# Kernel tuning notes

Hardware: AMD Instinct MI355X
Metric: run time of the kernel (lower is better)

The kernel has to match this reference:

```python
import jax, jax.numpy as jnp
import numpy as np
import math

IN_F, OUT_F = 4096, 4096
ORDER, TENSOR_RANK = 4, 8
LEAF_A = math.ceil(IN_F ** (1.0 / ORDER))   # 8
LEAF_B = math.ceil(OUT_F ** (1.0 / ORDER))  # 8


def setup_inputs() -> dict:
    key = jax.random.key(0)
    k1, k2, k3, k4 = jax.random.split(key, 4)
    x = jax.random.normal(k1, (8, 2048, IN_F), dtype=jnp.float32)
    weight = jax.random.normal(k2, (OUT_F, IN_F), dtype=jnp.float32) * 0.02
    bias = jax.random.normal(k3, (OUT_F,), dtype=jnp.float32) * 0.02
    # reset_parameters: gain for leaky_relu(sqrt(5)) = sqrt(2/(1+5)); std = gain / in_features**(1/order)
    gain = math.sqrt(2.0 / (1.0 + 5.0))
    std = gain / (IN_F ** (1.0 / ORDER))
    weight_leafs = jax.random.uniform(
        k4, (ORDER, TENSOR_RANK, LEAF_A, LEAF_B), dtype=jnp.float32,
        minval=-std, maxval=std)
    return {"x": x, "weight": weight, "bias": bias, "weight_leafs": weight_leafs}


def _reproduce_weight(weight_leafs):
    # Original einsum 'lij,rmn->rimjn' sums the FIRST operand over its leading
    # (rank) axis; chained through both stages + final .sum(0), every leaf is
    # summed over tensor_rank. Exact math = nested Kronecker of the rank-summed
    # leaves, sliced to [:in_features, :out_features].
    s = weight_leafs.sum(axis=1)  # (4, a, b)
    a, b = LEAF_A, LEAF_B
    z1 = jnp.einsum('ij,mn->imjn', s[0], s[1]).reshape(a * a, b * b)
    z2 = jnp.einsum('ij,mn->imjn', s[2], s[3]).reshape(a * a, b * b)
    zzz = jnp.einsum('ij,mn->imjn', z1, z2).reshape(a ** 4, b ** 4)
    return zzz[:IN_F, :OUT_F]  # (in_features, out_features)


def reference(x, weight, bias, weight_leafs):
    tensor_weight = _reproduce_weight(weight_leafs)       # (in, out)
    full_weight = weight + tensor_weight.T                # (out, in)
    # F.linear: x @ W^T + b
    return jnp.einsum('bsi,oi->bso', x, full_weight) + bias
```

## Files before the change

### kernel.cpp

```cpp
#include <hip/hip_runtime.h>
#include <hip/hip_bf16.h>
#include <stdint.h>

typedef __attribute__((ext_vector_type(8)))  __bf16 bf16x8;
typedef __attribute__((ext_vector_type(4)))  float  f32x4;
typedef __attribute__((ext_vector_type(16))) float  f32x16;

#define IN_F   4096
#define OUT_F  4096
#define M_ROWS 16384

static __device__ __forceinline__ unsigned short f2bf(float f) {
    unsigned int u = __float_as_uint(f);
    u += 0x7FFFu + ((u >> 16) & 1u);
    return (unsigned short)(u >> 16);
}

#define PREP_WBLK 1366
#define PREP_NBLK 4096

__global__ __launch_bounds__(256) void prep_kernel(
    const float* __restrict__ weight, const float* __restrict__ leafs,
    const float* __restrict__ x,
    unsigned short* __restrict__ wb, unsigned short* __restrict__ xbuf)
{
    const int t = threadIdx.x;
    if (blockIdx.x < PREP_WBLK) {
        __shared__ float s[4][8][8];
        {
            const int o = t >> 6, a = (t >> 3) & 7, b = t & 7;
            float acc = 0.f;
            #pragma unroll
            for (int r = 0; r < 8; ++r)
                acc += leafs[o * 512 + r * 64 + a * 8 + b];
            s[o][a][b] = acc;
        }
        __syncthreads();

        const int total = (OUT_F * IN_F) / 8;
        for (int idx = blockIdx.x * 256 + t; idx < total; idx += PREP_WBLK * 256) {
            const int n  = idx >> 9;
            const int kg = idx & 511;
            const int n0 = n >> 9, n1 = (n >> 6) & 7, n2 = (n >> 3) & 7, n3 = n & 7;
            const int k0 = kg >> 6, k1 = (kg >> 3) & 7, k2 = kg & 7;
            const float p = s[0][k0][n0] * s[1][k1][n1] * s[2][k2][n2];
            const float4* wp = (const float4*)(weight + (size_t)n * IN_F + kg * 8);
            const float4 w0 = wp[0], w1 = wp[1];
            const float wv[8] = {w0.x, w0.y, w0.z, w0.w, w1.x, w1.y, w1.z, w1.w};
            unsigned int pk[4];
            #pragma unroll
            for (int j = 0; j < 4; ++j) {
                unsigned int lo = f2bf(wv[2*j]   + p * s[3][2*j]  [n3]);
                unsigned int hi = f2bf(wv[2*j+1] + p * s[3][2*j+1][n3]);
                pk[j] = lo | (hi << 16);
            }
            *reinterpret_cast<uint4*>(wb + (size_t)n * IN_F + kg * 8) =
                make_uint4(pk[0], pk[1], pk[2], pk[3]);
        }
    } else {
        const long long n8 = (long long)M_ROWS * IN_F / 8;
        const int xblocks = PREP_NBLK - PREP_WBLK;
        for (long long idx = (long long)(blockIdx.x - PREP_WBLK) * 256 + t;
             idx < n8; idx += (long long)xblocks * 256) {
            const float4* xp = (const float4*)(x + idx * 8);
            const float4 a = xp[0], b = xp[1];
            const float v[8] = {a.x, a.y, a.z, a.w, b.x, b.y, b.z, b.w};
            unsigned int pk[4];
            #pragma unroll
            for (int j = 0; j < 4; ++j)
                pk[j] = (unsigned int)f2bf(v[2*j]) | ((unsigned int)f2bf(v[2*j+1]) << 16);
            *reinterpret_cast<uint4*>(xbuf + idx * 8) =
                make_uint4(pk[0], pk[1], pk[2], pk[3]);
        }
    }
}

#define BK 64
#define NT 64

#define GLL(src, dst) __builtin_amdgcn_global_load_lds( \
    (const __attribute__((address_space(1))) void*)(src), \
    (__attribute__((address_space(3))) void*)(dst), 16, 0, 0)

#define SB0  __builtin_amdgcn_sched_barrier(0)
#define BAR  __builtin_amdgcn_s_barrier()
#define PRI1 __builtin_amdgcn_s_setprio(1)
#define PRI0 __builtin_amdgcn_s_setprio(0)
#define WLG0 asm volatile("s_waitcnt lgkmcnt(0)" ::: "memory")
#define WVM0 asm volatile("s_waitcnt vmcnt(0)" ::: "memory")

#define STAGE_A(b, h, ko) do { \
    GLL(pA[h] + (ko),             ldsb + (b)*32768 + (h)*16384 + t*16); \
    GLL(pA[h] + 64*IN_F + (ko),   ldsb + (b)*32768 + (h)*16384 + t*16 + 8192); } while(0)
#define STAGE_B(b, h, ko) do { \
    GLL(pB[h] + (ko),             ldsb + 65536 + (b)*32768 + (h)*16384 + t*16); \
    GLL(pB[h] + 64*IN_F + (ko),   ldsb + 65536 + (b)*32768 + (h)*16384 + t*16 + 8192); } while(0)

#define ARD(Q, KH) do { _Pragma("unroll") \
    for (int i_ = 0; i_ < 2; ++i_) { _Pragma("unroll") \
    for (int j_ = 0; j_ < 2; ++j_) \
        aF[i_][j_] = *(const bf16x8*)(aPan + ((Q)*2 + i_)*4096 + \
                     (aOff ^ ((((KH)*2 + j_)) << 5))); } } while(0)
#define BRD(KH) do { _Pragma("unroll") \
    for (int n_ = 0; n_ < 2; ++n_) { _Pragma("unroll") \
    for (int j_ = 0; j_ < 2; ++j_) \
        bFr[n_][j_] = *(const bf16x8*)(bPan + n_*4096 + \
                      (bOff ^ ((((KH)*2 + j_)) << 5))); } } while(0)
#define MM32(Q) do { _Pragma("unroll") \
    for (int i_ = 0; i_ < 2; ++i_) { _Pragma("unroll") \
    for (int n_ = 0; n_ < 2; ++n_) { _Pragma("unroll") \
    for (int j_ = 0; j_ < 2; ++j_) \
        acc[(Q)*2 + i_][n_] = __builtin_amdgcn_mfma_f32_32x32x16_bf16( \
            aF[i_][j_], bFr[n_][j_], acc[(Q)*2 + i_][n_], 0, 0, 0); } } } while(0)

#define TILE32(BUF, KO, PF) do { \
    const char* aPan = ldsb + (BUF)*32768 + wr*16384; \
    const char* bPan = ldsb + 65536 + (BUF)*32768 + (wcn >> 1)*16384; \
     \
    ARD(0, 0); BRD(0); \
    if (PF) { STAGE_A((BUF)^1, 0, KO); STAGE_A((BUF)^1, 1, KO); } \
    BAR; WLG0; SB0; PRI1; MM32(0); PRI0; BAR; \
     \
    ARD(1, 0); \
    if (PF) { STAGE_B((BUF)^1, 0, KO); STAGE_B((BUF)^1, 1, KO); } \
    BAR; WLG0; SB0; PRI1; MM32(1); PRI0; BAR; \
     \
    ARD(0, 1); BRD(1); \
    BAR; WLG0; SB0; PRI1; MM32(0); PRI0; BAR; \
     \
    ARD(1, 1); \
    BAR; WLG0; SB0; PRI1; MM32(1); PRI0; \
    if (PF) { WVM0; } \
    BAR; \
} while (0)

__global__ __launch_bounds__(512, 2) void gemm32_kernel(
    const unsigned short* __restrict__ xb,
    const unsigned short* __restrict__ wb,
    const float* __restrict__ bias,
    float* __restrict__ out)
{
    __shared__ unsigned short lds_us[65536];
    char* const ldsb = (char*)lds_us;

    const int t    = threadIdx.x;
    const int wave = t >> 6;
    const int lane = t & 63;
    const int ln31 = lane & 31;
    const int lhi  = lane >> 5;
    const int wr   = wave >> 2;
    const int wcn  = wave & 3;

    const int bid  = blockIdx.x;
    const int swzb = (bid & 7) * 128 + (bid >> 3);
    const int bm   = (swzb >> 4) * 256;
    const int bn   = (swzb & 15) * 256;

    const int r1  = t >> 3;
    const int slp = (t & 7) ^ (r1 & 7);
    const unsigned short* pA[2] = {
        xb + (size_t)(bm + r1) * IN_F + slp * 8,
        xb + (size_t)(bm + 128 + r1) * IN_F + slp * 8 };
    const unsigned short* pB[2] = {
        wb + (size_t)(bn + r1) * IN_F + slp * 8,
        wb + (size_t)(bn + 128 + r1) * IN_F + slp * 8 };

    const int c0   = ((lhi ^ (ln31 & 7)) << 4);
    const int aOff = ln31 * 128 + c0;
    const int bOff = ((wcn & 1) * 64 + ln31) * 128 + c0;

    f32x16 acc[4][2] = {};
    bf16x8 aF[2][2], bFr[2][2];

    STAGE_A(0, 0, 0); STAGE_A(0, 1, 0); STAGE_B(0, 0, 0); STAGE_B(0, 1, 0);
    WVM0; BAR;

    #pragma unroll 1
    for (int tt = 0; tt < NT - 2; tt += 2) {
        TILE32(0, (tt + 1) * BK, true);
        TILE32(1, (tt + 2) * BK, true);
    }
    TILE32(0, (NT - 1) * BK, true);
    TILE32(1, 0, false);

    #pragma unroll
    for (int fn = 0; fn < 2; ++fn) {
        const int col = bn + wcn * 64 + fn * 32 + ln31;
        const float bv = bias[col];
        #pragma unroll
        for (int fm = 0; fm < 4; ++fm) {
            const int rb = bm + wr * 128 + fm * 32 + 4 * lhi;
            #pragma unroll
            for (int reg = 0; reg < 16; ++reg) {
                const int row = rb + (reg & 3) + 8 * (reg >> 2);
                out[(size_t)row * OUT_F + col] = acc[fm][fn][reg] + bv;
            }
        }
    }
}

#define FBM 128
#define FBN 128
#define FBK 32

__global__ __launch_bounds__(256) void gemm_fb_kernel(
    const float* __restrict__ xf,
    const unsigned short* __restrict__ wb,
    const float* __restrict__ bias,
    float* __restrict__ out)
{
    __shared__ unsigned short As[FBM * FBK];
    __shared__ unsigned short Bs[FBN * FBK];

    const int t    = threadIdx.x;
    const int wave = t >> 6;
    const int lane = t & 63;
    const int lr   = lane & 15;
    const int kq   = lane >> 4;
    const int wr   = wave >> 1;
    const int wc   = wave & 1;

    const int bm = blockIdx.x * FBM;
    const int bn = blockIdx.y * FBN;
    const int srow = t >> 2;
    const int scol = (t & 3) * 8;

    f32x4 acc[4][4] = {};

    for (int kt = 0; kt < IN_F; kt += FBK) {
        #pragma unroll
        for (int g = 0; g < 2; ++g) {
            const int row = srow + g * 64;
            const float4* xp = (const float4*)(xf + (size_t)(bm + row) * IN_F + kt + scol);
            const float4 a0 = xp[0], a1 = xp[1];
            const float v[8] = {a0.x, a0.y, a0.z, a0.w, a1.x, a1.y, a1.z, a1.w};
            unsigned int pk[4];
            #pragma unroll
            for (int j = 0; j < 4; ++j)
                pk[j] = (unsigned int)f2bf(v[2*j]) | ((unsigned int)f2bf(v[2*j+1]) << 16);
            *reinterpret_cast<uint4*>(&As[row * FBK + scol]) =
                make_uint4(pk[0], pk[1], pk[2], pk[3]);
        }
        {
            const unsigned short* gb0 = wb + (size_t)(bn + srow) * IN_F + kt + scol;
            const unsigned short* gb1 = gb0 + (size_t)64 * IN_F;
            GLL(gb0, Bs + srow * FBK + scol);
            GLL(gb1, Bs + (64 + srow) * FBK + scol);
        }
        __syncthreads();

        bf16x8 af[4], bfr[4];
        #pragma unroll
        for (int m = 0; m < 4; ++m)
            af[m] = *reinterpret_cast<const bf16x8*>(As + (wr * 64 + m * 16 + lr) * FBK + kq * 8);
        #pragma unroll
        for (int n = 0; n < 4; ++n)
            bfr[n] = *reinterpret_cast<const bf16x8*>(Bs + (wc * 64 + n * 16 + lr) * FBK + kq * 8);

        #pragma unroll
        for (int m = 0; m < 4; ++m)
            #pragma unroll
            for (int n = 0; n < 4; ++n)
                acc[m][n] = __builtin_amdgcn_mfma_f32_16x16x32_bf16(af[m], bfr[n], acc[m][n], 0, 0, 0);

        __syncthreads();
    }

    const int crow0 = kq * 4;
    #pragma unroll
    for (int n = 0; n < 4; ++n) {
        const int col = bn + wc * 64 + n * 16 + lr;
        const float bv = bias[col];
        #pragma unroll
        for (int m = 0; m < 4; ++m) {
            const int rowb = bm + wr * 64 + m * 16 + crow0;
            #pragma unroll
            for (int j = 0; j < 4; ++j)
                out[(size_t)(rowb + j) * OUT_F + col] = acc[m][n][j] + bv;
        }
    }
}

extern "C" void kernel_launch(void* const* d_in, const int* in_sizes, int n_in,
                              void* d_out, int out_size, void* d_ws, size_t ws_size,
                              hipStream_t stream) {
    const float* x      = (const float*)d_in[0];
    const float* weight = (const float*)d_in[1];
    const float* bias   = (const float*)d_in[2];
    const float* leafs  = (const float*)d_in[3];
    float* out = (float*)d_out;

    unsigned short* wb = (unsigned short*)d_ws;
    unsigned short* xbuf = (unsigned short*)((char*)d_ws +
                           (size_t)OUT_F * IN_F * sizeof(unsigned short));

    const size_t need_full = (size_t)OUT_F * IN_F * 2 + (size_t)M_ROWS * IN_F * 2;
    const bool full = ws_size >= need_full;

    if (full) {
        prep_kernel<<<dim3(PREP_NBLK), dim3(256), 0, stream>>>(
            weight, leafs, x, wb, xbuf);
        gemm32_kernel<<<dim3((M_ROWS / 256) * (OUT_F / 256)), dim3(512), 0, stream>>>(
            xbuf, wb, bias, out);
    } else {
        prep_kernel<<<dim3(PREP_WBLK), dim3(256), 0, stream>>>(
            weight, leafs, x, wb, xbuf);
        gemm_fb_kernel<<<dim3(M_ROWS / FBM, OUT_F / FBN), dim3(256), 0, stream>>>(
            x, wb, bias, out);
    }
}
```

Baseline: 616.1 us.

## Restructure bf16 GEMM main loop around K-slab LDS layout with one barrier per tile

Replaces the hand-scheduled TILE32 pipeline with a simpler double-buffered loop. That loop used XOR-swizzled LDS panels, several barriers per tile and explicit waitcnt and sched barriers. The new loop stores each 64-wide K tile as four 16-element K slabs (32 bytes per row) and issues the next tile's global-to-LDS loads up front. It then runs 4 K-steps of 4x2 MFMAs with only one __syncthreads per tile. The aim is to cut barrier and scheduling overhead and simplify LDS fragment addressing. The cost is that global loads now fetch only 32 contiguous bytes per row, and overlap relies on the compiler's implicit waits instead of explicit vmcnt control.

```diff
diff --git a/kernel.cpp b/kernel.cpp
--- a/kernel.cpp
+++ b/kernel.cpp
@@ -82,59 +82,13 @@
     (const __attribute__((address_space(1))) void*)(src), \
     (__attribute__((address_space(3))) void*)(dst), 16, 0, 0)
 
-#define SB0  __builtin_amdgcn_sched_barrier(0)
-#define BAR  __builtin_amdgcn_s_barrier()
-#define PRI1 __builtin_amdgcn_s_setprio(1)
-#define PRI0 __builtin_amdgcn_s_setprio(0)
-#define WLG0 asm volatile("s_waitcnt lgkmcnt(0)" ::: "memory")
-#define WVM0 asm volatile("s_waitcnt vmcnt(0)" ::: "memory")
-
-#define STAGE_A(b, h, ko) do { \
-    GLL(pA[h] + (ko),             ldsb + (b)*32768 + (h)*16384 + t*16); \
-    GLL(pA[h] + 64*IN_F + (ko),   ldsb + (b)*32768 + (h)*16384 + t*16 + 8192); } while(0)
-#define STAGE_B(b, h, ko) do { \
-    GLL(pB[h] + (ko),             ldsb + 65536 + (b)*32768 + (h)*16384 + t*16); \
-    GLL(pB[h] + 64*IN_F + (ko),   ldsb + 65536 + (b)*32768 + (h)*16384 + t*16 + 8192); } while(0)
-
-#define ARD(Q, KH) do { _Pragma("unroll") \
-    for (int i_ = 0; i_ < 2; ++i_) { _Pragma("unroll") \
-    for (int j_ = 0; j_ < 2; ++j_) \
-        aF[i_][j_] = *(const bf16x8*)(aPan + ((Q)*2 + i_)*4096 + \
-                     (aOff ^ ((((KH)*2 + j_)) << 5))); } } while(0)
-#define BRD(KH) do { _Pragma("unroll") \
-    for (int n_ = 0; n_ < 2; ++n_) { _Pragma("unroll") \
-    for (int j_ = 0; j_ < 2; ++j_) \
-        bFr[n_][j_] = *(const bf16x8*)(bPan + n_*4096 + \
-                      (bOff ^ ((((KH)*2 + j_)) << 5))); } } while(0)
-#define MM32(Q) do { _Pragma("unroll") \
-    for (int i_ = 0; i_ < 2; ++i_) { _Pragma("unroll") \
-    for (int n_ = 0; n_ < 2; ++n_) { _Pragma("unroll") \
-    for (int j_ = 0; j_ < 2; ++j_) \
-        acc[(Q)*2 + i_][n_] = __builtin_amdgcn_mfma_f32_32x32x16_bf16( \
-            aF[i_][j_], bFr[n_][j_], acc[(Q)*2 + i_][n_], 0, 0, 0); } } } while(0)
-
-#define TILE32(BUF, KO, PF) do { \
-    const char* aPan = ldsb + (BUF)*32768 + wr*16384; \
-    const char* bPan = ldsb + 65536 + (BUF)*32768 + (wcn >> 1)*16384; \
-     \
-    ARD(0, 0); BRD(0); \
-    if (PF) { STAGE_A((BUF)^1, 0, KO); STAGE_A((BUF)^1, 1, KO); } \
-    BAR; WLG0; SB0; PRI1; MM32(0); PRI0; BAR; \
-     \
-    ARD(1, 0); \
-    if (PF) { STAGE_B((BUF)^1, 0, KO); STAGE_B((BUF)^1, 1, KO); } \
-    BAR; WLG0; SB0; PRI1; MM32(1); PRI0; BAR; \
-     \
-    ARD(0, 1); BRD(1); \
-    BAR; WLG0; SB0; PRI1; MM32(0); PRI0; BAR; \
-     \
-    ARD(1, 1); \
-    BAR; WLG0; SB0; PRI1; MM32(1); PRI0; \
-    if (PF) { WVM0; } \
-    BAR; \
-} while (0)
-
-__global__ __launch_bounds__(512, 2) void gemm32_kernel(
+#define STAGE(P, KO) do { _Pragma("unroll") \
+    for (int i_ = 0; i_ < 4; ++i_) { \
+        GLL(srcA + (KO) + i_ * 16, ldsb + (P)*65536 + t*16 + i_*8192); \
+        GLL(srcB + (KO) + i_ * 16, ldsb + (P)*65536 + 32768 + t*16 + i_*8192); \
+    } } while (0)
+
+__global__ __launch_bounds__(512, 2) void gemm32k_kernel(
     const unsigned short* __restrict__ xb,
     const unsigned short* __restrict__ wb,
     const float* __restrict__ bias,
@@ -156,32 +110,45 @@
     const int bm   = (swzb >> 4) * 256;
     const int bn   = (swzb & 15) * 256;
 
-    const int r1  = t >> 3;
-    const int slp = (t & 7) ^ (r1 & 7);
-    const unsigned short* pA[2] = {
-        xb + (size_t)(bm + r1) * IN_F + slp * 8,
-        xb + (size_t)(bm + 128 + r1) * IN_F + slp * 8 };
-    const unsigned short* pB[2] = {
-        wb + (size_t)(bn + r1) * IN_F + slp * 8,
-        wb + (size_t)(bn + 128 + r1) * IN_F + slp * 8 };
-
-    const int c0   = ((lhi ^ (ln31 & 7)) << 4);
-    const int aOff = ln31 * 128 + c0;
-    const int bOff = ((wcn & 1) * 64 + ln31) * 128 + c0;
+    const unsigned short* srcA =
+        xb + (size_t)(bm + ((t >> 1) & 255)) * IN_F + (t & 1) * 8;
+    const unsigned short* srcB =
+        wb + (size_t)(bn + ((t >> 1) & 255)) * IN_F + (t & 1) * 8;
+
+    const int aOff = (wr * 128 + ln31) * 32 + lhi * 16;
+    const int bOff = 32768 + (wcn * 64 + ln31) * 32 + lhi * 16;
 
     f32x16 acc[4][2] = {};
-    bf16x8 aF[2][2], bFr[2][2];
-
-    STAGE_A(0, 0, 0); STAGE_A(0, 1, 0); STAGE_B(0, 0, 0); STAGE_B(0, 1, 0);
-    WVM0; BAR;
+
+    STAGE(0, 0);
+    __syncthreads();
 
     #pragma unroll 1
-    for (int tt = 0; tt < NT - 2; tt += 2) {
-        TILE32(0, (tt + 1) * BK, true);
-        TILE32(1, (tt + 2) * BK, true);
-    }
-    TILE32(0, (NT - 1) * BK, true);
-    TILE32(1, 0, false);
+    for (int tt = 0; tt < NT; ++tt) {
+        const int p = tt & 1;
+        if (tt + 1 < NT) STAGE(p ^ 1, (tt + 1) * BK);
+
+        const char* pan = ldsb + p * 65536;
+        __builtin_amdgcn_s_setprio(1);
+        #pragma unroll
+        for (int ks = 0; ks < 4; ++ks) {
+            bf16x8 a[4], b[2];
+            #pragma unroll
+            for (int m = 0; m < 4; ++m)
+                a[m] = *(const bf16x8*)(pan + ks * 8192 + aOff + m * 1024);
+            #pragma unroll
+            for (int n = 0; n < 2; ++n)
+                b[n] = *(const bf16x8*)(pan + ks * 8192 + bOff + n * 1024);
+            #pragma unroll
+            for (int m = 0; m < 4; ++m)
+                #pragma unroll
+                for (int n = 0; n < 2; ++n)
+                    acc[m][n] = __builtin_amdgcn_mfma_f32_32x32x16_bf16(
+                        a[m], b[n], acc[m][n], 0, 0, 0);
+        }
+        __builtin_amdgcn_s_setprio(0);
+        __syncthreads();
+    }
 
     #pragma unroll
     for (int fn = 0; fn < 2; ++fn) {
@@ -300,7 +267,7 @@
     if (full) {
         prep_kernel<<<dim3(PREP_NBLK), dim3(256), 0, stream>>>(
             weight, leafs, x, wb, xbuf);
-        gemm32_kernel<<<dim3((M_ROWS / 256) * (OUT_F / 256)), dim3(512), 0, stream>>>(
+        gemm32k_kernel<<<dim3((M_ROWS / 256) * (OUT_F / 256)), dim3(512), 0, stream>>>(
             xbuf, wb, bias, out);
     } else {
         prep_kernel<<<dim3(PREP_WBLK), dim3(256), 0, stream>>>(
```

Measured after the change: 782.0 us. +26.9%, slower.
